# Kernel tuning notes

Hardware: AMD Instinct MI355X
Metric: run time of the kernel (lower is better)

## Reference

```python
import jax, jax.numpy as jnp
import numpy as np

D_MODEL = 1024
NUM_HEADS = 16
HEAD_DIM = D_MODEL // NUM_HEADS


def setup_inputs() -> dict:
    key = jax.random.key(0)
    ks = jax.random.split(key, 11)
    B, S = 2, 2048
    scale = 1.0 / np.sqrt(D_MODEL)
    inp = {
        "query": jax.random.normal(ks[0], (B, S, D_MODEL), jnp.float32),
        "key": jax.random.normal(ks[1], (B, S, D_MODEL), jnp.float32),
        "value": jax.random.normal(ks[2], (B, S, D_MODEL), jnp.float32),
        "Wq": jax.random.normal(ks[3], (D_MODEL, D_MODEL), jnp.float32) * scale,
        "bq": jnp.zeros((D_MODEL,), jnp.float32),
        "Wk": jax.random.normal(ks[4], (D_MODEL, D_MODEL), jnp.float32) * scale,
        "bk": jnp.zeros((D_MODEL,), jnp.float32),
        "Wv": jax.random.normal(ks[5], (D_MODEL, D_MODEL), jnp.float32) * scale,
        "bv": jnp.zeros((D_MODEL,), jnp.float32),
        "Wo": jax.random.normal(ks[6], (D_MODEL, D_MODEL), jnp.float32) * scale,
        "bo": jnp.zeros((D_MODEL,), jnp.float32),
    }
    return inp


def _split_heads(x):
    # [B, S, D] -> [B, H, S, Dh]
    B, S, _ = x.shape
    return x.reshape(B, S, NUM_HEADS, HEAD_DIM).transpose(0, 2, 1, 3)


def reference(query, key, value, Wq, bq, Wk, bk, Wv, bv, Wo, bo):
    q = _split_heads(query @ Wq.T + bq)   # [B,H,S,Dh]
    k = _split_heads(key @ Wk.T + bk)
    v = _split_heads(value @ Wv.T + bv)
    scores = jnp.einsum('bhqd,bhkd->bhqk', q, k) / jnp.sqrt(
        jnp.asarray(HEAD_DIM, q.dtype))
    probs = jax.nn.softmax(scores, axis=-1)
    ctx = jnp.einsum('bhqk,bhkd->bhqd', probs, v)  # [B,H,S,Dh]
    B, H, S, Dh = ctx.shape
    ctx = ctx.transpose(0, 2, 1, 3).reshape(B, S, H * Dh)  # [B,S,D]
    return ctx @ Wo.T + bo
```

## Files before the change

kernel.cpp:

```cpp
#include <hip/hip_runtime.h>
#include <hip/hip_bf16.h>
#include <stdint.h>

#define D_MODEL 1024
#define NHEADS  16
#define HDIM    64
#define BATCH   2
#define SEQ     2048
#define MROWS   (BATCH*SEQ)

typedef __attribute__((ext_vector_type(8))) short  bf16x8;
typedef __attribute__((ext_vector_type(4))) float  f32x4;
typedef __attribute__((ext_vector_type(4))) int    int4v;

__device__ __forceinline__ unsigned short f2bf(float f) {
  unsigned int u = __float_as_uint(f);
  u = (u + 0x7fffu + ((u >> 16) & 1u)) >> 16;
  return (unsigned short)u;
}

__device__ __forceinline__ unsigned cvtpk_bf16(float lo, float hi) {
  unsigned r;
  asm("v_cvt_pk_bf16_f32 %0, %1, %2" : "=v"(r) : "v"(lo), "v"(hi));
  return r;
}

__device__ __forceinline__ void gload_lds16(const unsigned short* g, unsigned short* l) {
  __builtin_amdgcn_global_load_lds(
      (const __attribute__((address_space(1))) void*)g,
      (__attribute__((address_space(3))) void*)l,
      16, 0, 0);
}

__device__ __forceinline__ int swz_chunk(int row) { return (row + (row >> 3)) & 7; }
__device__ __forceinline__ int kperm(int m) {
  return (m & 0x63) | ((m & 0x10) >> 2) | ((m & 0x0C) << 1);
}

struct CvtArgs {
  const float* src[7];
  unsigned short* dst[7];
  int n[7];
};

__global__ __launch_bounds__(256) void cvt_all(CvtArgs a) {
  int t = blockIdx.y;
  const float* s = a.src[t];
  unsigned short* d = a.dst[t];
  int n = a.n[t];
  int stride = gridDim.x * blockDim.x * 4;
  for (int i = (blockIdx.x * blockDim.x + threadIdx.x) * 4; i < n; i += stride) {
    float4 v = *(const float4*)(s + i);
    ushort4 o;
    o.x = f2bf(v.x); o.y = f2bf(v.y); o.z = f2bf(v.z); o.w = f2bf(v.w);
    *(ushort4*)(d + i) = o;
  }
}

__device__ __forceinline__ void gemm_core(const unsigned short* __restrict__ X,
                                          const unsigned short* __restrict__ W,
                                          int m0, int n0,
                                          unsigned short* As, unsigned short* Bs,
                                          f32x4 (&acc)[4][4]) {
  const int tid  = threadIdx.x;
  const int lane = tid & 63;
  const int wv   = tid >> 6;
  const int wr   = wv >> 1, wc = wv & 1;
  const int srow = tid >> 3;
  const int scol = (((tid & 7) ^ (srow & 7)) * 8);
  const int sdst = tid * 16;

  for (int kt = 0; kt < D_MODEL / 64; ++kt) {
    __syncthreads();
    const unsigned short* Xs = X + (size_t)m0 * D_MODEL + kt * 64;
    const unsigned short* Ws = W + (size_t)n0 * D_MODEL + kt * 64;
#pragma unroll
    for (int c = 0; c < 4; ++c) {
      gload_lds16(Xs + (size_t)(srow + c * 32) * D_MODEL + scol,
                  (unsigned short*)((char*)As + sdst + c * 4096));
      gload_lds16(Ws + (size_t)(srow + c * 32) * D_MODEL + scol,
                  (unsigned short*)((char*)Bs + sdst + c * 4096));
    }
    __syncthreads();
#pragma unroll
    for (int kc = 0; kc < 2; ++kc) {
      bf16x8 af[4], bfv[4];
#pragma unroll
      for (int i = 0; i < 4; ++i) {
        int arow  = wr * 64 + i * 16 + (lane & 15);
        int abyte = (arow * 128 + (kc * 32 + 8 * (lane >> 4)) * 2) ^ ((arow & 7) << 4);
        af[i] = *(const bf16x8*)((const char*)As + abyte);
        int brow  = wc * 64 + i * 16 + (lane & 15);
        int bbyte = (brow * 128 + (kc * 32 + 8 * (lane >> 4)) * 2) ^ ((brow & 7) << 4);
        bfv[i] = *(const bf16x8*)((const char*)Bs + bbyte);
      }
#pragma unroll
      for (int mi = 0; mi < 4; ++mi)
#pragma unroll
        for (int ni = 0; ni < 4; ++ni)
          acc[mi][ni] = __builtin_amdgcn_mfma_f32_16x16x32_bf16(af[mi], bfv[ni],
                                                                acc[mi][ni], 0, 0, 0);
    }
  }
}

__global__ __launch_bounds__(256) void gemm_qkv(
    const unsigned short* __restrict__ Xq, const unsigned short* __restrict__ Xk,
    const unsigned short* __restrict__ Xv,
    const unsigned short* __restrict__ Wq, const unsigned short* __restrict__ Wk,
    const unsigned short* __restrict__ Wv,
    const float* __restrict__ bq, const float* __restrict__ bk,
    const float* __restrict__ bv,
    unsigned short* __restrict__ oq, unsigned short* __restrict__ ok,
    unsigned short* __restrict__ ov) {
  __shared__ __align__(16) unsigned short As[128 * 64];
  __shared__ __align__(16) unsigned short Bs[128 * 64];
  int z = blockIdx.z;
  const unsigned short* X = (z == 0) ? Xq : (z == 1) ? Xk : Xv;
  const unsigned short* W = (z == 0) ? Wq : (z == 1) ? Wk : Wv;
  const float* bias       = (z == 0) ? bq : (z == 1) ? bk : bv;
  unsigned short* out     = (z == 0) ? oq : (z == 1) ? ok : ov;
  float scale = (z == 0) ? 0.18033688011112042f : 1.0f;

  int m0 = blockIdx.y * 128, n0 = blockIdx.x * 128;
  f32x4 acc[4][4] = {};
  gemm_core(X, W, m0, n0, As, Bs, acc);

  const int lane = threadIdx.x & 63;
  const int wv   = threadIdx.x >> 6;
  const int wr   = wv >> 1, wc = wv & 1;
#pragma unroll
  for (int mi = 0; mi < 4; ++mi)
#pragma unroll
    for (int ni = 0; ni < 4; ++ni)
#pragma unroll
      for (int r = 0; r < 4; ++r) {
        int m = m0 + wr * 64 + mi * 16 + (lane >> 4) * 4 + r;
        int n = n0 + wc * 64 + ni * 16 + (lane & 15);
        float val = (acc[mi][ni][r] + bias[n]) * scale;
        int b = m >> 11, s = m & 2047;
        int h = n >> 6, dh = n & 63;
        out[(((size_t)(b * NHEADS + h)) * SEQ + s) * HDIM + dh] = f2bf(val);
      }
}

__global__ __launch_bounds__(256) void gemm_out(
    const unsigned short* __restrict__ Xc, const unsigned short* __restrict__ Wo,
    const float* __restrict__ bo, float* __restrict__ out) {
  __shared__ __align__(16) unsigned short As[128 * 64];
  __shared__ __align__(16) unsigned short Bs[128 * 64];
  int m0 = blockIdx.y * 128, n0 = blockIdx.x * 128;
  f32x4 acc[4][4] = {};
  gemm_core(Xc, Wo, m0, n0, As, Bs, acc);

  const int lane = threadIdx.x & 63;
  const int wv   = threadIdx.x >> 6;
  const int wr   = wv >> 1, wc = wv & 1;
#pragma unroll
  for (int mi = 0; mi < 4; ++mi)
#pragma unroll
    for (int ni = 0; ni < 4; ++ni)
#pragma unroll
      for (int r = 0; r < 4; ++r) {
        int m = m0 + wr * 64 + mi * 16 + (lane >> 4) * 4 + r;
        int n = n0 + wc * 64 + ni * 16 + (lane & 15);
        out[(size_t)m * D_MODEL + n] = acc[mi][ni][r] + bo[n];
      }
}

__global__ __launch_bounds__(256) void transpose_v(
    const unsigned short* __restrict__ vs, unsigned short* __restrict__ vt) {
  __shared__ __align__(16) unsigned short T[64 * 64];
  int st = blockIdx.x, bh = blockIdx.y;
  const unsigned short* src = vs + ((size_t)bh * SEQ + st * 64) * HDIM;
  int tid = threadIdx.x;
  int d0 = (tid & 7) * 8;
#pragma unroll
  for (int c = 0; c < 2; ++c) {
    int s = (tid >> 3) + c * 32;
    bf16x8 vv = *(const bf16x8*)(src + (size_t)s * HDIM + d0);
    const unsigned short* e = (const unsigned short*)&vv;
#pragma unroll
    for (int j = 0; j < 8; ++j) {
      int row = d0 + j;
      int byte = row * 128 + ((s * 2) ^ (swz_chunk(row) << 4));
      *(unsigned short*)((char*)T + byte) = e[j];
    }
  }
  __syncthreads();
  int d  = tid >> 2;
  int c0 = (tid & 3) * 2;
  int sw = swz_chunk(d);
  bf16x8 o0 = *(const bf16x8*)((const char*)T + d * 128 + ((c0 ^ sw) << 4));
  bf16x8 o1 = *(const bf16x8*)((const char*)T + d * 128 + (((c0 + 1) ^ sw) << 4));
  unsigned short* dst = vt + ((size_t)bh * HDIM + d) * SEQ + st * 64 + c0 * 8;
  *(bf16x8*)(dst)     = o0;
  *(bf16x8*)(dst + 8) = o1;
}

__global__ __launch_bounds__(256, 2) void attn(
    const unsigned short* __restrict__ q, const unsigned short* __restrict__ k,
    const unsigned short* __restrict__ vt, unsigned short* __restrict__ ctx) {
  __shared__ __align__(16) unsigned short K0[128 * 64], V0[64 * 128];
  __shared__ __align__(16) unsigned short K1[128 * 64], V1[64 * 128];

  const int tid  = threadIdx.x;
  const int lane = tid & 63;
  const int wv   = tid >> 6;
  const int g    = lane >> 4;
  const int cl   = lane & 15;

  const int bh = blockIdx.x;
  const int qt = blockIdx.y;

  const unsigned short* qb  = q  + (size_t)bh * SEQ * HDIM;
  const unsigned short* kb  = k  + (size_t)bh * SEQ * HDIM;
  const unsigned short* vbt = vt + (size_t)bh * HDIM * SEQ;

  bf16x8 qf[2][2];
  {
    int qbase = qt * 128 + wv * 32;
#pragma unroll
    for (int qh = 0; qh < 2; ++qh) {
      const unsigned short* qp = qb + (size_t)(qbase + qh * 16 + cl) * HDIM + 8 * g;
      qf[qh][0] = *(const bf16x8*)(qp);
      qf[qh][1] = *(const bf16x8*)(qp + 32);
    }
  }

  const int srowK = tid >> 3;
  const int swzK  = swz_chunk(srowK);
  const int vrow  = tid >> 4;
  const int swzV  = swz_chunk(vrow);
  const int ldst  = tid * 16;

  f32x4 acc0[4] = {}, acc1[4] = {};
  f32x4 accs0 = {}, accs1 = {};
  const int4v onesi = {0x3F803F80, 0x3F803F80, 0x3F803F80, 0x3F803F80};
  const bf16x8 onesb = __builtin_bit_cast(bf16x8, onesi);
  const float FIXED_M = 12.0f;

  auto stageK_ = [&](int t, unsigned short* Kb) {
    const unsigned short* kt_ = kb + (size_t)t * 128 * HDIM;
#pragma unroll
    for (int c = 0; c < 4; ++c) {
      int row  = srowK + 32 * c;
      int col  = ((tid & 7) ^ swzK ^ ((c & 1) << 2)) * 8;
      gload_lds16(kt_ + (size_t)kperm(row) * HDIM + col,
                  (unsigned short*)((char*)Kb + ldst + c * 4096));
    }
  };
  auto stageV_ = [&](int t, unsigned short* Vb) {
    const unsigned short* vt_ = vbt + t * 128;
#pragma unroll
    for (int c = 0; c < 4; ++c) {
      int row = vrow + 16 * c;
      int sw  = (swzV + 2 * c) & 7;
      int col = (((tid & 7) ^ sw) | (tid & 8)) * 8;
      gload_lds16(vt_ + (size_t)row * SEQ + col,
                  (unsigned short*)((char*)Vb + ldst + c * 4096));
    }
  };

  f32x4 sc[8][2];

  auto qk = [&](const unsigned short* Kb) {
#pragma unroll
    for (int ni = 0; ni < 8; ++ni) { sc[ni][0] = f32x4{}; sc[ni][1] = f32x4{}; }
    __builtin_amdgcn_s_setprio(1);
#pragma unroll
    for (int kc = 0; kc < 2; ++kc)
#pragma unroll
      for (int ni = 0; ni < 8; ++ni) {
        int row  = ni * 16 + cl;
        int byte = row * 128 + (((kc * 4 + g) ^ swz_chunk(row)) << 4);
        bf16x8 kf = *(const bf16x8*)((const char*)Kb + byte);
        sc[ni][0] = __builtin_amdgcn_mfma_f32_16x16x32_bf16(kf, qf[0][kc], sc[ni][0], 0, 0, 0);
        sc[ni][1] = __builtin_amdgcn_mfma_f32_16x16x32_bf16(kf, qf[1][kc], sc[ni][1], 0, 0, 0);
      }
    __builtin_amdgcn_s_setprio(0);
  };

  auto smpack = [&](int4v (&pa0)[4], int4v (&pa1)[4]) {
#pragma unroll
    for (int qh = 0; qh < 2; ++qh)
#pragma unroll
      for (int ni = 0; ni < 8; ++ni)
#pragma unroll
        for (int r = 0; r < 4; ++r)
          sc[ni][qh][r] = __builtin_amdgcn_exp2f(sc[ni][qh][r] - FIXED_M);
#pragma unroll
    for (int kcp = 0; kcp < 4; ++kcp) {
      pa0[kcp][0] = (int)cvtpk_bf16(sc[2 * kcp][0][0], sc[2 * kcp][0][1]);
      pa0[kcp][1] = (int)cvtpk_bf16(sc[2 * kcp][0][2], sc[2 * kcp][0][3]);
      pa0[kcp][2] = (int)cvtpk_bf16(sc[2 * kcp + 1][0][0], sc[2 * kcp + 1][0][1]);
      pa0[kcp][3] = (int)cvtpk_bf16(sc[2 * kcp + 1][0][2], sc[2 * kcp + 1][0][3]);
      pa1[kcp][0] = (int)cvtpk_bf16(sc[2 * kcp][1][0], sc[2 * kcp][1][1]);
      pa1[kcp][1] = (int)cvtpk_bf16(sc[2 * kcp][1][2], sc[2 * kcp][1][3]);
      pa1[kcp][2] = (int)cvtpk_bf16(sc[2 * kcp + 1][1][0], sc[2 * kcp + 1][1][1]);
      pa1[kcp][3] = (int)cvtpk_bf16(sc[2 * kcp + 1][1][2], sc[2 * kcp + 1][1][3]);
    }
  };

  auto pv = [&](const unsigned short* Vb, int4v (&pa0)[4], int4v (&pa1)[4]) {
    __builtin_amdgcn_s_setprio(1);
#pragma unroll
    for (int kcp = 0; kcp < 4; ++kcp) {
      bf16x8 a0 = __builtin_bit_cast(bf16x8, pa0[kcp]);
      bf16x8 a1 = __builtin_bit_cast(bf16x8, pa1[kcp]);
#pragma unroll
      for (int nd = 0; nd < 4; ++nd) {
        int row = nd * 16 + cl;
        int c   = kcp * 4 + g;
        int byte = row * 256 + ((((c & 7) ^ swz_chunk(row)) | (c & 8)) << 4);
        bf16x8 vf = *(const bf16x8*)((const char*)Vb + byte);
        acc0[nd] = __builtin_amdgcn_mfma_f32_16x16x32_bf16(a0, vf, acc0[nd], 0, 0, 0);
        acc1[nd] = __builtin_amdgcn_mfma_f32_16x16x32_bf16(a1, vf, acc1[nd], 0, 0, 0);
      }
      accs0 = __builtin_amdgcn_mfma_f32_16x16x32_bf16(a0, onesb, accs0, 0, 0, 0);
      accs1 = __builtin_amdgcn_mfma_f32_16x16x32_bf16(a1, onesb, accs1, 0, 0, 0);
    }
    __builtin_amdgcn_s_setprio(0);
  };

  const int NT = SEQ / 128;
  stageK_(0, K0);
  stageV_(0, V0);
  __syncthreads();
  stageK_(1, K1);
  qk(K0);
  for (int i = 0; i < NT; ++i) {
    int4v pa0[4], pa1[4];
    smpack(pa0, pa1);
    __syncthreads();
    if (i + 2 < NT) stageK_(i + 2, (i & 1) ? K1 : K0);
    if (i + 1 < NT) stageV_(i + 1, (i & 1) ? V0 : V1);
    if (i + 1 < NT) qk((i & 1) ? K0 : K1);
    pv((i & 1) ? V1 : V0, pa0, pa1);
  }

  int b = bh >> 4, h = bh & 15;
#pragma unroll
  for (int r = 0; r < 4; ++r) {
    float i0 = 1.0f / accs0[r];
    float i1 = 1.0f / accs1[r];
#pragma unroll
    for (int qh = 0; qh < 2; ++qh) {
      int srow_o = qt * 128 + wv * 32 + qh * 16 + g * 4 + r;
      float iv = qh ? i1 : i0;
#pragma unroll
      for (int nd = 0; nd < 4; ++nd) {
        int d = nd * 16 + cl;
        float val = (qh ? acc1[nd][r] : acc0[nd][r]) * iv;
        ctx[(((size_t)(b * SEQ + srow_o)) * NHEADS + h) * HDIM + d] = f2bf(val);
      }
    }
  }
}

extern "C" void kernel_launch(void* const* d_in, const int* in_sizes, int n_in,
                              void* d_out, int out_size, void* d_ws, size_t ws_size,
                              hipStream_t stream) {
  (void)in_sizes; (void)n_in; (void)out_size; (void)ws_size;
  const float* query = (const float*)d_in[0];
  const float* key_  = (const float*)d_in[1];
  const float* value = (const float*)d_in[2];
  const float* Wq = (const float*)d_in[3];
  const float* bq = (const float*)d_in[4];
  const float* Wk = (const float*)d_in[5];
  const float* bk = (const float*)d_in[6];
  const float* Wv = (const float*)d_in[7];
  const float* bv = (const float*)d_in[8];
  const float* Wo = (const float*)d_in[9];
  const float* bo = (const float*)d_in[10];
  float* out = (float*)d_out;

  unsigned short* w = (unsigned short*)d_ws;
  const size_t NA = (size_t)MROWS * D_MODEL;
  const size_t NW = (size_t)D_MODEL * D_MODEL;
  unsigned short* Xq  = w;
  unsigned short* Xk  = Xq + NA;
  unsigned short* Xv  = Xk + NA;
  unsigned short* Wqb = Xv + NA;
  unsigned short* Wkb = Wqb + NW;
  unsigned short* Wvb = Wkb + NW;
  unsigned short* Wob = Wvb + NW;
  unsigned short* qs  = Wob + NW;
  unsigned short* ks  = qs + NA;
  unsigned short* vs  = ks + NA;
  unsigned short* cx  = vs + NA;
  unsigned short* vtb = Xq;

  CvtArgs ca;
  ca.src[0] = query; ca.dst[0] = Xq;  ca.n[0] = (int)NA;
  ca.src[1] = key_;  ca.dst[1] = Xk;  ca.n[1] = (int)NA;
  ca.src[2] = value; ca.dst[2] = Xv;  ca.n[2] = (int)NA;
  ca.src[3] = Wq;    ca.dst[3] = Wqb; ca.n[3] = (int)NW;
  ca.src[4] = Wk;    ca.dst[4] = Wkb; ca.n[4] = (int)NW;
  ca.src[5] = Wv;    ca.dst[5] = Wvb; ca.n[5] = (int)NW;
  ca.src[6] = Wo;    ca.dst[6] = Wob; ca.n[6] = (int)NW;

  cvt_all<<<dim3(256, 7, 1), 256, 0, stream>>>(ca);
  gemm_qkv<<<dim3(8, 32, 3), 256, 0, stream>>>(Xq, Xk, Xv, Wqb, Wkb, Wvb,
                                               bq, bk, bv, qs, ks, vs);
  transpose_v<<<dim3(32, 32, 1), 256, 0, stream>>>(vs, vtb);
  attn<<<dim3(32, 16, 1), 256, 0, stream>>>(qs, ks, vtb, cx);
  gemm_out<<<dim3(8, 32, 1), 256, 0, stream>>>(cx, Wob, bo, out);
}
```

Baseline: 131.1 us.

## Replace QKV projection with 256x256-tile triple-buffered pipelined GEMM kernel

Swaps the 128x128 QKV GEMM for a 512-thread kernel computing 256x256 tiles with K-step 32, using a three-slot LDS ring fed by direct global-to-LDS loads. Loads for later stages are issued in the middle of MFMA phases, and waits are done with explicit vmcnt counts and barriers, with raised wave priority around the MFMA blocks. Block IDs are remapped across the 192 tiles to group blocks that share inputs, aiming for better cache reuse. The larger tile raises arithmetic intensity per LDS byte, but 192 blocks on 256 CUs leaves some CUs idle and the hand-written wait counts are fragile.

```diff
diff --git a/kernel.cpp b/kernel.cpp
--- a/kernel.cpp
+++ b/kernel.cpp
@@ -33,6 +33,7 @@
 }
 
 __device__ __forceinline__ int swz_chunk(int row) { return (row + (row >> 3)) & 7; }
+__device__ __forceinline__ int swz4(int row) { return (row + (row >> 2)) & 3; }
 __device__ __forceinline__ int kperm(int m) {
   return (m & 0x63) | ((m & 0x10) >> 2) | ((m & 0x0C) << 1);
 }
@@ -55,6 +56,131 @@
     o.x = f2bf(v.x); o.y = f2bf(v.y); o.z = f2bf(v.z); o.w = f2bf(v.w);
     *(ushort4*)(d + i) = o;
   }
+}
+
+__global__ __launch_bounds__(512, 2) void gemm_qkv256(
+    const unsigned short* __restrict__ Xq, const unsigned short* __restrict__ Xk,
+    const unsigned short* __restrict__ Xv,
+    const unsigned short* __restrict__ Wq, const unsigned short* __restrict__ Wk,
+    const unsigned short* __restrict__ Wv,
+    const float* __restrict__ bq, const float* __restrict__ bk,
+    const float* __restrict__ bv,
+    unsigned short* __restrict__ oq, unsigned short* __restrict__ ok,
+    unsigned short* __restrict__ ov) {
+  __shared__ __align__(16) unsigned short LDS[3 * 16384];
+
+  const int tid  = threadIdx.x;
+  const int lane = tid & 63;
+  const int w8   = tid >> 6;
+  const int wr   = w8 >> 2;
+  const int wc   = w8 & 3;
+  const int g    = lane >> 4;
+  const int cl   = lane & 15;
+
+  int fid = blockIdx.x;
+  int sid = (fid & 7) * 24 + (fid >> 3);
+  int ny = sid / 12, nx = sid % 12;
+  int z  = nx >> 2;
+  int n0 = (nx & 3) * 256;
+  int m0 = ny * 256;
+
+  const unsigned short* X = (z == 0) ? Xq : (z == 1) ? Xk : Xv;
+  const unsigned short* W = (z == 0) ? Wq : (z == 1) ? Wk : Wv;
+  const float* bias       = (z == 0) ? bq : (z == 1) ? bk : bv;
+  unsigned short* outp    = (z == 0) ? oq : (z == 1) ? ok : ov;
+  float scale = (z == 0) ? 0.18033688011112042f : 1.0f;
+
+  const int srow   = tid >> 2;
+  const int schunk = tid & 3;
+  const int scol   = (schunk ^ swz4(srow)) * 8;
+
+  auto stageH = [&](int h) {
+    if (h >= 64) return;
+    int t_ = h >> 1, qa = h & 1;
+    unsigned short* buf = LDS + (t_ % 3) * 16384 + qa * 8192;
+    const unsigned short* src = qa ? (W + (size_t)(n0 + srow) * D_MODEL)
+                                   : (X + (size_t)(m0 + srow) * D_MODEL);
+    src += t_ * 32 + scol;
+    gload_lds16(src,                          buf + tid * 8);
+    gload_lds16(src + (size_t)128 * D_MODEL,  buf + 4096 + tid * 8);
+  };
+
+  f32x4 acc[8][4] = {};
+
+  stageH(0); stageH(1); stageH(2); stageH(3);
+  asm volatile("s_waitcnt vmcnt(4)" ::: "memory");
+  __builtin_amdgcn_s_barrier();
+  __builtin_amdgcn_sched_barrier(0);
+
+  for (int t = 0; t < 32; ++t) {
+    const unsigned short* Ab = LDS + (t % 3) * 16384;
+    const unsigned short* Bb = Ab + 8192;
+    bf16x8 af[4], bcache[4];
+
+#pragma unroll
+    for (int i = 0; i < 4; ++i) {
+      int row = wr * 128 + i * 16 + cl;
+      af[i] = *(const bf16x8*)((const char*)Ab + row * 64 + ((g ^ swz4(row)) << 4));
+    }
+#pragma unroll
+    for (int j = 0; j < 4; ++j) {
+      int row = wc * 64 + j * 16 + cl;
+      bcache[j] = *(const bf16x8*)((const char*)Bb + row * 64 + ((g ^ swz4(row)) << 4));
+    }
+    stageH(2 * t + 4);
+    __builtin_amdgcn_s_barrier();
+    __builtin_amdgcn_sched_barrier(0);
+    __builtin_amdgcn_s_setprio(1);
+#pragma unroll
+    for (int i = 0; i < 4; ++i)
+#pragma unroll
+      for (int j = 0; j < 4; ++j)
+        acc[i][j] = __builtin_amdgcn_mfma_f32_16x16x32_bf16(af[i], bcache[j],
+                                                            acc[i][j], 0, 0, 0);
+    __builtin_amdgcn_s_setprio(0);
+    __builtin_amdgcn_s_barrier();
+    __builtin_amdgcn_sched_barrier(0);
+
+#pragma unroll
+    for (int i = 0; i < 4; ++i) {
+      int row = wr * 128 + (4 + i) * 16 + cl;
+      af[i] = *(const bf16x8*)((const char*)Ab + row * 64 + ((g ^ swz4(row)) << 4));
+    }
+    stageH(2 * t + 5);
+    __builtin_amdgcn_s_barrier();
+    __builtin_amdgcn_sched_barrier(0);
+    __builtin_amdgcn_s_setprio(1);
+#pragma unroll
+    for (int i = 0; i < 4; ++i)
+#pragma unroll
+      for (int j = 0; j < 4; ++j)
+        acc[4 + i][j] = __builtin_amdgcn_mfma_f32_16x16x32_bf16(af[i], bcache[j],
+                                                                acc[4 + i][j], 0, 0, 0);
+    __builtin_amdgcn_s_setprio(0);
+    if (t < 30) {
+      asm volatile("s_waitcnt vmcnt(4)" ::: "memory");
+    } else if (t == 30) {
+      asm volatile("s_waitcnt vmcnt(0)" ::: "memory");
+    }
+    __builtin_amdgcn_s_barrier();
+    __builtin_amdgcn_sched_barrier(0);
+  }
+
+#pragma unroll
+  for (int mi = 0; mi < 8; ++mi)
+#pragma unroll
+    for (int nj = 0; nj < 4; ++nj) {
+      int n = n0 + wc * 64 + nj * 16 + cl;
+      float bn = bias[n];
+      int h = n >> 6, dh = n & 63;
+#pragma unroll
+      for (int r = 0; r < 4; ++r) {
+        int m = m0 + wr * 128 + mi * 16 + g * 4 + r;
+        float val = (acc[mi][nj][r] + bn) * scale;
+        int b = m >> 11, s = m & 2047;
+        outp[(((size_t)(b * NHEADS + h)) * SEQ + s) * HDIM + dh] = f2bf(val);
+      }
+    }
 }
 
 __device__ __forceinline__ void gemm_core(const unsigned short* __restrict__ X,
@@ -102,46 +228,6 @@
                                                                 acc[mi][ni], 0, 0, 0);
     }
   }
-}
-
-__global__ __launch_bounds__(256) void gemm_qkv(
-    const unsigned short* __restrict__ Xq, const unsigned short* __restrict__ Xk,
-    const unsigned short* __restrict__ Xv,
-    const unsigned short* __restrict__ Wq, const unsigned short* __restrict__ Wk,
-    const unsigned short* __restrict__ Wv,
-    const float* __restrict__ bq, const float* __restrict__ bk,
-    const float* __restrict__ bv,
-    unsigned short* __restrict__ oq, unsigned short* __restrict__ ok,
-    unsigned short* __restrict__ ov) {
-  __shared__ __align__(16) unsigned short As[128 * 64];
-  __shared__ __align__(16) unsigned short Bs[128 * 64];
-  int z = blockIdx.z;
-  const unsigned short* X = (z == 0) ? Xq : (z == 1) ? Xk : Xv;
-  const unsigned short* W = (z == 0) ? Wq : (z == 1) ? Wk : Wv;
-  const float* bias       = (z == 0) ? bq : (z == 1) ? bk : bv;
-  unsigned short* out     = (z == 0) ? oq : (z == 1) ? ok : ov;
-  float scale = (z == 0) ? 0.18033688011112042f : 1.0f;
-
-  int m0 = blockIdx.y * 128, n0 = blockIdx.x * 128;
-  f32x4 acc[4][4] = {};
-  gemm_core(X, W, m0, n0, As, Bs, acc);
-
-  const int lane = threadIdx.x & 63;
-  const int wv   = threadIdx.x >> 6;
-  const int wr   = wv >> 1, wc = wv & 1;
-#pragma unroll
-  for (int mi = 0; mi < 4; ++mi)
-#pragma unroll
-    for (int ni = 0; ni < 4; ++ni)
-#pragma unroll
-      for (int r = 0; r < 4; ++r) {
-        int m = m0 + wr * 64 + mi * 16 + (lane >> 4) * 4 + r;
-        int n = n0 + wc * 64 + ni * 16 + (lane & 15);
-        float val = (acc[mi][ni][r] + bias[n]) * scale;
-        int b = m >> 11, s = m & 2047;
-        int h = n >> 6, dh = n & 63;
-        out[(((size_t)(b * NHEADS + h)) * SEQ + s) * HDIM + dh] = f2bf(val);
-      }
 }
 
 __global__ __launch_bounds__(256) void gemm_out(
@@ -401,8 +487,8 @@
   ca.src[6] = Wo;    ca.dst[6] = Wob; ca.n[6] = (int)NW;
 
   cvt_all<<<dim3(256, 7, 1), 256, 0, stream>>>(ca);
-  gemm_qkv<<<dim3(8, 32, 3), 256, 0, stream>>>(Xq, Xk, Xv, Wqb, Wkb, Wvb,
-                                               bq, bk, bv, qs, ks, vs);
+  gemm_qkv256<<<dim3(192, 1, 1), 512, 0, stream>>>(Xq, Xk, Xv, Wqb, Wkb, Wvb,
+                                                   bq, bk, bv, qs, ks, vs);
   transpose_v<<<dim3(32, 32, 1), 256, 0, stream>>>(vs, vtb);
   attn<<<dim3(32, 16, 1), 256, 0, stream>>>(qs, ks, vtb, cx);
   gemm_out<<<dim3(8, 32, 1), 256, 0, stream>>>(cx, Wob, bo, out);
```

Result: faster. 123.4 us (-5.9%).
